# Kernel optimization log

Measured on AMD Instinct MI355X. Metric: run time of the kernel, lower is better.

## Reference

```python
import jax, jax.numpy as jnp
import numpy as np

DIM = 1024
HEADS = 16
HEAD_DIM = DIM // HEADS
K_NEIGH = 64  # local_window, adaptive_window=False
SCALE = 1.0 / np.sqrt(HEAD_DIM)


def setup_inputs() -> dict:
    key = jax.random.key(0)
    ks = jax.random.split(key, 6)
    b, n = 1, 4096
    x = jax.random.normal(ks[0], (b, n, DIM), dtype=jnp.float32)
    cantor_coords = jax.random.uniform(ks[1], (n,), dtype=jnp.float32)
    # torch nn.Linear(dim, 3*dim): weight [3*dim, dim]; we store transposed [dim, 3*dim]
    W_qkv = jax.random.normal(ks[2], (DIM, 3 * DIM), dtype=jnp.float32) * (1.0 / np.sqrt(DIM))
    b_qkv = jax.random.normal(ks[3], (3 * DIM,), dtype=jnp.float32) * 0.01
    W_out = jax.random.normal(ks[4], (DIM, DIM), dtype=jnp.float32) * (1.0 / np.sqrt(DIM))
    b_out = jax.random.normal(ks[5], (DIM,), dtype=jnp.float32) * 0.01
    return {"x": x, "cantor_coords": cantor_coords, "W_qkv": W_qkv,
            "b_qkv": b_qkv, "W_out": W_out, "b_out": b_out}


def _routes(cantor_coords):
    # [n, n] pairwise |c_i - c_j|; k smallest -> top_k of negated distances
    d = jnp.abs(cantor_coords[:, None] - cantor_coords[None, :])
    _, idx = jax.lax.top_k(-d, K_NEIGH)  # [n, k]
    return idx


def reference(x, cantor_coords, W_qkv, b_qkv, W_out, b_out):
    b, n, _ = x.shape
    qkv = x @ W_qkv + b_qkv                          # [b, n, 3*dim]
    qkv = qkv.reshape(b, n, 3, HEADS, HEAD_DIM)
    qkv = jnp.transpose(qkv, (2, 0, 3, 1, 4))        # [3, b, h, n, d]
    q, k, v = qkv[0], qkv[1], qkv[2]

    routes = _routes(cantor_coords)                  # [n, k]
    k_g = k[:, :, routes, :]                         # [b, h, n, k, d]
    v_g = v[:, :, routes, :]
    scores = jnp.einsum('bhqd,bhqkd->bhqk', q, k_g) * SCALE
    attn = jax.nn.softmax(scores, axis=-1)           # dropout p=0 (eval)
    out = jnp.einsum('bhqk,bhqkd->bhqd', attn, v_g)  # [b, h, n, d]
    out = jnp.transpose(out, (0, 2, 1, 3)).reshape(b, n, DIM)
    return out @ W_out + b_out
```

## Files before the change

### kernel.cpp

```cpp
#include <hip/hip_runtime.h>
#include <hip/hip_bf16.h>

typedef _Float16 f16x8 __attribute__((ext_vector_type(8)));
typedef float f32x4 __attribute__((ext_vector_type(4)));
typedef unsigned long long u64;

#define NSEQ 4096
#define DIMM 1024
#define NQKV 3072

#define BAR() asm volatile("s_barrier" ::: "memory")

__device__ __forceinline__ f32x4 mfma16(f16x8 a, f16x8 b, f32x4 c) {
  return __builtin_amdgcn_mfma_f32_16x16x32_f16(a, b, c, 0, 0, 0);
}

__device__ __forceinline__ void glds16(const void* g, void* l) {
  __builtin_amdgcn_global_load_lds(
      (const __attribute__((address_space(1))) void*)g,
      (__attribute__((address_space(3))) void*)l, 16, 0, 0);
}

__global__ __launch_bounds__(256) void prep_kernel(
    const float* __restrict__ x, _Float16* __restrict__ xh,
    const float* __restrict__ Wqkv, _Float16* __restrict__ wqkvt,
    const float* __restrict__ Wout, _Float16* __restrict__ woutt,
    const float* __restrict__ cc, int* __restrict__ sorted_idx,
    float* __restrict__ csort) {
  __shared__ __align__(16) char plds[16640];
  const int bid = blockIdx.x, t = threadIdx.x;
  if (bid < 2048) {
    const int i = bid * 256 + t;
    const float4 a = ((const float4*)x)[i * 2];
    const float4 b = ((const float4*)x)[i * 2 + 1];
    f16x8 o = {(_Float16)a.x, (_Float16)a.y, (_Float16)a.z, (_Float16)a.w,
               (_Float16)b.x, (_Float16)b.y, (_Float16)b.z, (_Float16)b.w};
    ((f16x8*)xh)[i] = o;
  } else if (bid < 3072) {
    const bool qkv = bid < 2816;
    const int sub = qkv ? bid - 2048 : bid - 2816;
    const float* W = qkv ? Wqkv : Wout;
    _Float16* Wt = qkv ? wqkvt : woutt;
    const int Nn = qkv ? 3072 : 1024;
    const int k0 = (sub & 15) * 64, n0 = (sub >> 4) * 64;
    float (*tile)[65] = (float(*)[65])plds;
    const int tx = t & 63, ty = t >> 6;
    for (int rr = ty; rr < 64; rr += 4)
      tile[rr][tx] = W[(size_t)(k0 + rr) * Nn + n0 + tx];
    __syncthreads();
#pragma unroll
    for (int it = 0; it < 2; ++it) {
      const int idx = it * 256 + t;
      const int row = idx >> 3, seg = idx & 7;
      f16x8 v;
#pragma unroll
      for (int j = 0; j < 8; ++j) v[j] = (_Float16)tile[seg * 8 + j][row];
      *(f16x8*)&Wt[(size_t)(n0 + row) * 1024 + k0 + seg * 8] = v;
    }
  } else {
    float* sc = (float*)plds;
#pragma unroll
    for (int it = 0; it < 4; ++it) {
      const int i = it * 256 + t;
      ((float4*)sc)[i] = ((const float4*)cc)[i];
    }
    __syncthreads();
    const int elem = (bid - 3072) * 32 + (t >> 3);
    const int s = t & 7;
    const unsigned mybits = __float_as_uint(sc[elem]);
    int cnt = 0;
#pragma unroll 8
    for (int m = 0; m < 512; ++m) {
      const int j = s + (m << 3);
      const unsigned bj = __float_as_uint(sc[j]);
      cnt += (bj < mybits || (bj == mybits && j < elem)) ? 1 : 0;
    }
    cnt += __shfl_xor(cnt, 1);
    cnt += __shfl_xor(cnt, 2);
    cnt += __shfl_xor(cnt, 4);
    if (s == 0) {
      sorted_idx[cnt] = elem;
      csort[cnt] = sc[elem];
    }
  }
}

__device__ __forceinline__ f16x8 ldsfrag(const char* base, int r, int g) {
  return *(const f16x8*)(base + r * 128 + ((g ^ (r & 7)) << 4));
}

__device__ __forceinline__ void stage_half(const char* gbase, size_t kb, int t,
                                           char* lds_half, int tid) {
#pragma unroll
  for (int s = 0; s < 2; ++s) {
    const int rel = tid * 16 + s * 8192;
    const int r = rel >> 7;
    const int g = (rel >> 4) & 7;
    const int gg = g ^ (r & 7);
    glds16(gbase + (size_t)r * kb + t * 128 + gg * 16, lds_half + rel);
  }
}

__device__ __forceinline__ void stage_64r(const char* gbase, size_t kb, int t,
                                          char* lds8k, int tid) {
  const int rel = tid * 16;
  const int r = rel >> 7;
  const int g = (rel >> 4) & 7;
  const int gg = g ^ (r & 7);
  glds16(gbase + (size_t)r * kb + t * 128 + gg * 16, lds8k + rel);
}

__device__ __forceinline__ void rd_b3(const char* Bb, int wn, int lr, int kg,
                                      f16x8 (&bf)[3][2]) {
#pragma unroll
  for (int nt = 0; nt < 3; ++nt) {
    bf[nt][0] = ldsfrag(Bb, wn + nt * 16 + lr, kg);
    bf[nt][1] = ldsfrag(Bb, wn + nt * 16 + lr, 4 + kg);
  }
}

template <int Q>
__device__ __forceinline__ void rd_a(const char* Ab, int wm, int lr, int kg,
                                     f16x8 (&af)[2][2]) {
#pragma unroll
  for (int m = 0; m < 2; ++m) {
    af[m][0] = ldsfrag(Ab, wm + (2 * Q + m) * 16 + lr, kg);
    af[m][1] = ldsfrag(Ab, wm + (2 * Q + m) * 16 + lr, 4 + kg);
  }
}

template <int Q>
__device__ __forceinline__ void do_mfma3(const f16x8 (&af)[2][2],
                                         const f16x8 (&bf)[3][2],
                                         f32x4 (&acc)[8][3]) {
#pragma unroll
  for (int m = 0; m < 2; ++m)
#pragma unroll
    for (int nt = 0; nt < 3; ++nt) {
      acc[2 * Q + m][nt] = mfma16(af[m][0], bf[nt][0], acc[2 * Q + m][nt]);
      acc[2 * Q + m][nt] = mfma16(af[m][1], bf[nt][1], acc[2 * Q + m][nt]);
    }
}

template <bool LAST>
__device__ __forceinline__ void ktile_pair192(const char* Ag, const char* Bg,
                                              size_t kb, char* smem, int tid,
                                              int wm, int wn, int lr, int kg,
                                              int t1, int t2, int t3,
                                              f32x4 (&acc)[8][3]) {
  char* A0 = smem;
  char* A1 = smem + 32768;
  char* B0 = smem + 65536;
  char* B1 = smem + 65536 + 24576;
  f16x8 bf[3][2], af[2][2];
  rd_b3(B0, wn, lr, kg, bf);
  rd_a<0>(A0, wm, lr, kg, af);
  stage_64r(Ag, kb, t1, A1, tid);
  stage_64r(Ag + 64 * kb, kb, t1, A1 + 8192, tid);
  BAR();
  __builtin_amdgcn_s_setprio(1);
  do_mfma3<0>(af, bf, acc);
  __builtin_amdgcn_s_setprio(0);
  BAR();
  rd_a<1>(A0, wm, lr, kg, af);
  stage_64r(Ag + 128 * kb, kb, t1, A1 + 16384, tid);
  stage_64r(Ag + 192 * kb, kb, t1, A1 + 24576, tid);
  BAR();
  __builtin_amdgcn_s_setprio(1);
  do_mfma3<1>(af, bf, acc);
  __builtin_amdgcn_s_setprio(0);
  BAR();
  rd_a<2>(A0, wm, lr, kg, af);
  if (!LAST) {
    stage_64r(Bg, kb, t2, B0, tid);
    stage_64r(Bg + 64 * kb, kb, t2, B0 + 8192, tid);
  }
  BAR();
  __builtin_amdgcn_s_setprio(1);
  do_mfma3<2>(af, bf, acc);
  __builtin_amdgcn_s_setprio(0);
  BAR();
  rd_a<3>(A0, wm, lr, kg, af);
  if (!LAST) stage_64r(Bg + 128 * kb, kb, t2, B0 + 16384, tid);
  BAR();
  __builtin_amdgcn_s_setprio(1);
  do_mfma3<3>(af, bf, acc);
  __builtin_amdgcn_s_setprio(0);
  if (LAST)
    asm volatile("s_waitcnt vmcnt(0)" ::: "memory");
  else
    asm volatile("s_waitcnt vmcnt(3)" ::: "memory");
  BAR();
  rd_b3(B1, wn, lr, kg, bf);
  rd_a<0>(A1, wm, lr, kg, af);
  if (!LAST) {
    stage_64r(Ag, kb, t2, A0, tid);
    stage_64r(Ag + 64 * kb, kb, t2, A0 + 8192, tid);
  }
  BAR();
  __builtin_amdgcn_s_setprio(1);
  do_mfma3<0>(af, bf, acc);
  __builtin_amdgcn_s_setprio(0);
  BAR();
  rd_a<1>(A1, wm, lr, kg, af);
  if (!LAST) {
    stage_64r(Ag + 128 * kb, kb, t2, A0 + 16384, tid);
    stage_64r(Ag + 192 * kb, kb, t2, A0 + 24576, tid);
  }
  BAR();
  __builtin_amdgcn_s_setprio(1);
  do_mfma3<1>(af, bf, acc);
  __builtin_amdgcn_s_setprio(0);
  BAR();
  rd_a<2>(A1, wm, lr, kg, af);
  if (!LAST) {
    stage_64r(Bg, kb, t3, B1, tid);
    stage_64r(Bg + 64 * kb, kb, t3, B1 + 8192, tid);
  }
  BAR();
  __builtin_amdgcn_s_setprio(1);
  do_mfma3<2>(af, bf, acc);
  __builtin_amdgcn_s_setprio(0);
  BAR();
  rd_a<3>(A1, wm, lr, kg, af);
  if (!LAST) stage_64r(Bg + 128 * kb, kb, t3, B1 + 16384, tid);
  BAR();
  __builtin_amdgcn_s_setprio(1);
  do_mfma3<3>(af, bf, acc);
  __builtin_amdgcn_s_setprio(0);
  if (!LAST) asm volatile("s_waitcnt vmcnt(3)" ::: "memory");
  BAR();
}

__global__ __launch_bounds__(512, 2) void qkvmask_kernel(
    const _Float16* __restrict__ A, const _Float16* __restrict__ Bt,
    const float* __restrict__ bias, _Float16* __restrict__ C,
    const float* __restrict__ csort, const int* __restrict__ sorted_idx,
    unsigned* __restrict__ masks) {
  extern __shared__ char smem[];
  const int tid = threadIdx.x;
  const int lane = tid & 63, wid = tid >> 6;
  if (blockIdx.x >= 256) {
    const int p = (blockIdx.x - 256) * 8 + wid;
    int W0 = 64 * (p >> 6) - 64;
    W0 = min(max(W0, 0), NSEQ - 192);
    const float cp = csort[p];
    u64 key[4];
#pragma unroll
    for (int r = 0; r < 3; ++r) {
      const int w = r * 64 + lane;
      const float d = fabsf(csort[W0 + w] - cp);
      key[r] = (((u64)__float_as_uint(d)) << 20) |
               (((u64)(unsigned)sorted_idx[W0 + w]) << 8) | (unsigned)w;
    }
    key[3] = ~0ull;
#pragma unroll
    for (int k = 2; k <= 256; k <<= 1) {
#pragma unroll
      for (int j = k >> 1; j > 0; j >>= 1) {
        if (j >= 64) {
          const int rj = j >> 6;
#pragma unroll
          for (int r = 0; r < 4; ++r) {
            const int rp = r ^ rj;
            if (rp > r) {
              const bool up = (((r * 64) & k) == 0);
              const u64 a = key[r], b2 = key[rp];
              const bool sw = (a > b2) == up;
              key[r] = sw ? b2 : a;
              key[rp] = sw ? a : b2;
            }
          }
        } else {
#pragma unroll
          for (int r = 0; r < 4; ++r) {
            const u64 pv = __shfl_xor(key[r], j);
            const bool up = (((r * 64 + lane) & k) == 0);
            const bool lower = ((lane & j) == 0);
            const bool takemin = (lower == up);
            const u64 mn = key[r] < pv ? key[r] : pv;
            const u64 mx = key[r] < pv ? pv : key[r];
            key[r] = takemin ? mn : mx;
          }
        }
      }
    }
    const unsigned w0 = (unsigned)(key[0] & 0xffu);
    const unsigned hi = w0 >> 5, bit = 1u << (w0 & 31u);
    unsigned m0w = hi == 0 ? bit : 0u;
    unsigned m1w = hi == 1 ? bit : 0u;
    unsigned m2w = hi == 2 ? bit : 0u;
    unsigned m3w = hi == 3 ? bit : 0u;
    unsigned m4w = hi == 4 ? bit : 0u;
    unsigned m5w = hi == 5 ? bit : 0u;
#pragma unroll
    for (int s = 1; s < 64; s <<= 1) {
      m0w |= __shfl_xor(m0w, s);
      m1w |= __shfl_xor(m1w, s);
      m2w |= __shfl_xor(m2w, s);
      m3w |= __shfl_xor(m3w, s);
      m4w |= __shfl_xor(m4w, s);
      m5w |= __shfl_xor(m5w, s);
    }
    if (lane < 8) {
      unsigned val = 0u;
      val = lane == 0 ? m0w : val;
      val = lane == 1 ? m1w : val;
      val = lane == 2 ? m2w : val;
      val = lane == 3 ? m3w : val;
      val = lane == 4 ? m4w : val;
      val = lane == 5 ? m5w : val;
      masks[p * 8 + lane] = val;
    }
    return;
  }
  const int NN = 3072;
  const size_t kb = 2048;
  const int lr = lane & 15, kg = lane >> 4;
  const int wm = (wid >> 2) * 128, wn = (wid & 3) * 48;
  const int bid = blockIdx.x;
  const int flat = (bid & 7) * 32 + (bid >> 3);
  const int bx = flat >> 4, by = flat & 15;
  const int m0 = bx * 256, n0 = by * 192;
  const char* Ag = (const char*)A + (size_t)m0 * kb;
  const char* Bg = (const char*)Bt + (size_t)n0 * kb;
  char* A0 = smem;
  char* B0 = smem + 65536;
  char* B1 = smem + 65536 + 24576;
  f32x4 acc[8][3] = {};
#pragma unroll
  for (int u = 0; u < 4; ++u)
    stage_64r(Ag + (size_t)(64 * u) * kb, kb, 0, A0 + u * 8192, tid);
#pragma unroll
  for (int u = 0; u < 3; ++u)
    stage_64r(Bg + (size_t)(64 * u) * kb, kb, 0, B0 + u * 8192, tid);
#pragma unroll
  for (int u = 0; u < 3; ++u)
    stage_64r(Bg + (size_t)(64 * u) * kb, kb, 1, B1 + u * 8192, tid);
  asm volatile("s_waitcnt vmcnt(3)" ::: "memory");
  BAR();
#pragma unroll 1
  for (int i = 0; i < 7; ++i)
    ktile_pair192<false>(Ag, Bg, kb, smem, tid, wm, wn, lr, kg, 2 * i + 1,
                         2 * i + 2, 2 * i + 3, acc);
  ktile_pair192<true>(Ag, Bg, kb, smem, tid, wm, wn, lr, kg, 15, 16, 17, acc);
#pragma unroll
  for (int nt = 0; nt < 3; ++nt) {
    const int col = n0 + wn + nt * 16 + lr;
    const float bv = bias[col];
#pragma unroll
    for (int mt = 0; mt < 8; ++mt) {
      const int row0 = m0 + wm + mt * 16 + kg * 4;
#pragma unroll
      for (int rr = 0; rr < 4; ++rr)
        C[(size_t)(row0 + rr) * NN + col] = (_Float16)(acc[mt][nt][rr] + bv);
    }
  }
}

__global__ __launch_bounds__(512, 2) void out_gemm128_kernel(
    const _Float16* __restrict__ A, const _Float16* __restrict__ Bt,
    const float* __restrict__ bias, float* __restrict__ C) {
  extern __shared__ char smem[];
  const size_t kb = 2048;
  const int tid = threadIdx.x;
  const int lane = tid & 63, wid = tid >> 6;
  const int lr = lane & 15, kg = lane >> 4;
  const int wm = (wid >> 2) * 64, wn = (wid & 3) * 32;
  const int bid = blockIdx.x;
  const int flat = (bid & 7) * 32 + (bid >> 3);
  const int bx = flat >> 3, by = flat & 7;
  const int m0 = bx * 128, n0 = by * 128;
  const char* Ag = (const char*)A + (size_t)m0 * kb;
  const char* Bg = (const char*)Bt + (size_t)n0 * kb;
  f32x4 acc[4][2] = {};
  stage_half(Ag, kb, 0, smem, tid);
  stage_half(Bg, kb, 0, smem + 49152, tid);
  stage_half(Ag, kb, 1, smem + 16384, tid);
  stage_half(Bg, kb, 1, smem + 49152 + 16384, tid);
  asm volatile("s_waitcnt vmcnt(4)" ::: "memory");
  BAR();
#pragma unroll
  for (int t = 0; t < 16; ++t) {
    const char* At = smem + (t % 3) * 16384;
    const char* Bb = smem + 49152 + (t % 3) * 16384;
    f16x8 bf[2][2], af[4][2];
#pragma unroll
    for (int nt = 0; nt < 2; ++nt) {
      bf[nt][0] = ldsfrag(Bb, wn + nt * 16 + lr, kg);
      bf[nt][1] = ldsfrag(Bb, wn + nt * 16 + lr, 4 + kg);
    }
#pragma unroll
    for (int m = 0; m < 4; ++m) {
      af[m][0] = ldsfrag(At, wm + m * 16 + lr, kg);
      af[m][1] = ldsfrag(At, wm + m * 16 + lr, 4 + kg);
    }
    if (t < 14) {
      stage_half(Ag, kb, t + 2, smem + ((t + 2) % 3) * 16384, tid);
      stage_half(Bg, kb, t + 2, smem + 49152 + ((t + 2) % 3) * 16384, tid);
    }
    BAR();
    __builtin_amdgcn_s_setprio(1);
#pragma unroll
    for (int m = 0; m < 4; ++m)
#pragma unroll
      for (int nt = 0; nt < 2; ++nt) {
        acc[m][nt] = mfma16(af[m][0], bf[nt][0], acc[m][nt]);
        acc[m][nt] = mfma16(af[m][1], bf[nt][1], acc[m][nt]);
      }
    __builtin_amdgcn_s_setprio(0);
    if (t < 14)
      asm volatile("s_waitcnt vmcnt(4)" ::: "memory");
    else if (t == 14)
      asm volatile("s_waitcnt vmcnt(0)" ::: "memory");
    BAR();
  }
#pragma unroll
  for (int nt = 0; nt < 2; ++nt) {
    const int col = n0 + wn + nt * 16 + lr;
    const float bv = bias[col];
#pragma unroll
    for (int mt = 0; mt < 4; ++mt) {
      const int row0 = m0 + wm + mt * 16 + kg * 4;
#pragma unroll
      for (int rr = 0; rr < 4; ++rr)
        C[(size_t)(row0 + rr) * 1024 + col] = acc[mt][nt][rr] + bv;
    }
  }
}

__global__ __launch_bounds__(256) void attn_kernel(
    const _Float16* __restrict__ qkvh, const unsigned* __restrict__ masks,
    const int* __restrict__ sorted_idx, _Float16* __restrict__ attn_h) {
  __shared__ __align__(128) char sK[24576];
  __shared__ __align__(128) char sV[24576];
  const int flat = (blockIdx.x & 7) * 128 + (blockIdx.x >> 3);
  const int b = flat & 63, h = flat >> 6;
  const int tid = threadIdx.x, lane = tid & 63, wid = tid >> 6;
  const int W0 = min(max(64 * b - 64, 0), NSEQ - 192);
  const int lrow16 = lane & 15, kgrp = lane >> 4;
  int ridx[6];
#pragma unroll
  for (int c = 0; c < 6; ++c)
    ridx[c] = sorted_idx[W0 + c * 32 + wid * 8 + (lane >> 3)];
#pragma unroll
  for (int c = 0; c < 6; ++c) {
    const int o = c * 4096 + wid * 1024 + lane * 16;
    const int row = o >> 7;
    const int inrow = (o & 127) ^ ((row & 7) << 4);
    glds16((const char*)qkvh + (size_t)ridx[c] * 6144 + 2048 + h * 128 + inrow,
           sK + o);
  }
  f16x8 vreg[6];
#pragma unroll
  for (int c = 0; c < 6; ++c) {
    const int o = c * 4096 + wid * 1024 + lane * 16;
    vreg[c] = *(const f16x8*)((const char*)qkvh + (size_t)ridx[c] * 6144 +
                              4096 + h * 128 + (o & 127));
  }
  const int p_base = b * 64 + wid * 16;
  const int orig_q = sorted_idx[p_base + lrow16];
  const char* qp = (const char*)qkvh + (size_t)orig_q * 6144 + h * 128 + kgrp * 16;
  const f16x8 aq0 = *(const f16x8*)qp;
  const f16x8 aq1 = *(const f16x8*)(qp + 64);
  unsigned mb[4];
#pragma unroll
  for (int r = 0; r < 4; ++r) {
    const int p = p_base + kgrp * 4 + r;
    const uint4 wa = *(const uint4*)&masks[p * 8];
    const uint2 wb2 = *(const uint2*)&masks[p * 8 + 4];
    const unsigned wsv6[6] = {wa.x, wa.y, wa.z, wa.w, wb2.x, wb2.y};
    unsigned bits = 0;
#pragma unroll
    for (int n = 0; n < 12; ++n)
      bits |= ((wsv6[n >> 1] >> (((n & 1) << 4) + lrow16)) & 1u) << n;
    mb[r] = bits;
  }
  const int lrot = lane & 7;
#pragma unroll
  for (int c = 0; c < 6; ++c) {
    const int o = c * 4096 + wid * 1024 + lane * 16;
    const int k = o >> 7;
    const int d0 = (o & 127) >> 1;
#pragma unroll
    for (int ee = 0; ee < 8; ++ee) {
      const int e = (ee + lrot) & 7;
      const int d = d0 + e;
      *(_Float16*)(sV + d * 384 + ((2 * k) ^ ((d & 7) << 4))) = vreg[c][e];
    }
  }
  __syncthreads();
  float sv[12][4];
#pragma unroll
  for (int n = 0; n < 12; ++n) {
    const int j = n * 16 + lrow16;
    const int sw = (j & 7) << 4;
    const char* kr = sK + j * 128;
    const f16x8 b0 = *(const f16x8*)(kr + ((kgrp * 16) ^ sw));
    const f16x8 b1 = *(const f16x8*)(kr + ((64 + kgrp * 16) ^ sw));
    f32x4 a = {};
    a = mfma16(aq0, b0, a);
    a = mfma16(aq1, b1, a);
#pragma unroll
    for (int r = 0; r < 4; ++r)
      sv[n][r] = ((mb[r] >> n) & 1u) ? a[r] * 0.125f : -1e30f;
  }
#pragma unroll
  for (int r = 0; r < 4; ++r) {
    float m = sv[0][r];
#pragma unroll
    for (int n = 1; n < 12; ++n) m = fmaxf(m, sv[n][r]);
    m = fmaxf(m, __shfl_xor(m, 1));
    m = fmaxf(m, __shfl_xor(m, 2));
    m = fmaxf(m, __shfl_xor(m, 4));
    m = fmaxf(m, __shfl_xor(m, 8));
    float s = 0.f;
#pragma unroll
    for (int n = 0; n < 12; ++n) {
      const float e = __expf(sv[n][r] - m);
      sv[n][r] = e;
      s += e;
    }
    s += __shfl_xor(s, 1);
    s += __shfl_xor(s, 2);
    s += __shfl_xor(s, 4);
    s += __shfl_xor(s, 8);
    const float rinv = 1.f / s;
#pragma unroll
    for (int n = 0; n < 12; ++n) sv[n][r] *= rinv;
  }
  __syncthreads();
#pragma unroll
  for (int n = 0; n < 12; ++n) {
#pragma unroll
    for (int r = 0; r < 4; ++r) {
      const int lrw = wid * 16 + kgrp * 4 + r;
      const int cb = (n * 16 + lrow16) * 2;
      *(_Float16*)(sK + lrw * 384 + (cb ^ ((lrw & 7) << 4))) = (_Float16)sv[n][r];
    }
  }
  __syncthreads();
  f32x4 oacc[4] = {};
  const int arow = wid * 16 + lrow16;
  const int swa = (arow & 7) << 4;
#pragma unroll
  for (int kt = 0; kt < 6; ++kt) {
    const int kbo = kt * 64 + kgrp * 16;
    const f16x8 pa = *(const f16x8*)(sK + arow * 384 + (kbo ^ swa));
#pragma unroll
    for (int nt = 0; nt < 4; ++nt) {
      const int d = nt * 16 + lrow16;
      const f16x8 vb = *(const f16x8*)(sV + d * 384 + (kbo ^ ((d & 7) << 4)));
      oacc[nt] = mfma16(pa, vb, oacc[nt]);
    }
  }
#pragma unroll
  for (int r = 0; r < 4; ++r) {
    const int p = p_base + kgrp * 4 + r;
    const int orig = sorted_idx[p];
    _Float16* op = attn_h + (size_t)orig * DIMM + h * 64;
#pragma unroll
    for (int nt = 0; nt < 4; ++nt)
      op[nt * 16 + lrow16] = (_Float16)oacc[nt][r];
  }
}

extern "C" void kernel_launch(void* const* d_in, const int* in_sizes, int n_in,
                              void* d_out, int out_size, void* d_ws, size_t ws_size,
                              hipStream_t stream) {
  const float* x = (const float*)d_in[0];
  const float* cc = (const float*)d_in[1];
  const float* Wqkv = (const float*)d_in[2];
  const float* bqkv = (const float*)d_in[3];
  const float* Wout = (const float*)d_in[4];
  const float* bout = (const float*)d_in[5];
  char* ws = (char*)d_ws;

  _Float16* xh = (_Float16*)(ws + 0);
  _Float16* wqkvt = (_Float16*)(ws + 8388608);
  _Float16* woutt = (_Float16*)(ws + 14680064);
  _Float16* qkvh = (_Float16*)(ws + 16777216);
  _Float16* atnh = (_Float16*)(ws + 41943040);
  int* sidx = (int*)(ws + 50331648);
  float* csort = (float*)(ws + 50348032);
  unsigned* msk = (unsigned*)(ws + 50364416);

  hipFuncSetAttribute((const void*)qkvmask_kernel,
                      hipFuncAttributeMaxDynamicSharedMemorySize, 114688);
  hipFuncSetAttribute((const void*)out_gemm128_kernel,
                      hipFuncAttributeMaxDynamicSharedMemorySize, 98304);

  prep_kernel<<<3200, 256, 0, stream>>>(x, xh, Wqkv, wqkvt, Wout, woutt, cc,
                                        sidx, csort);
  qkvmask_kernel<<<768, 512, 114688, stream>>>(xh, wqkvt, bqkv, qkvh, csort,
                                               sidx, msk);
  attn_kernel<<<1024, 256, 0, stream>>>(qkvh, msk, sidx, atnh);
  out_gemm128_kernel<<<256, 512, 98304, stream>>>(atnh, woutt, bout,
                                                  (float*)d_out);
}
```

Before: 102.0 us.

## Enlarge QKV GEMM tile to 256x256 and double per-block mask work

The QKV projection GEMM tile grows from 256x192 to 256x256, giving 192 GEMM blocks instead of 256, with each wave holding 8x4 accumulator tiles and B staged in 32 KB halves. The neighbour-mask blocks now process 16 positions each over two iterations, so 256 mask blocks replace 512 and the grid shrinks from 768 to 448. The aim is better arithmetic intensity per loaded byte and fewer block launches. In exchange, LDS per block rises to 128 KB, which may lower occupancy, and more accumulator registers are needed. 192 blocks may also underfill the GPU's compute units.

```diff
diff --git a/kernel.cpp b/kernel.cpp
--- a/kernel.cpp
+++ b/kernel.cpp
@@ -101,27 +101,18 @@
   }
 }
 
-__device__ __forceinline__ void stage_64r(const char* gbase, size_t kb, int t,
-                                          char* lds8k, int tid) {
-  const int rel = tid * 16;
-  const int r = rel >> 7;
-  const int g = (rel >> 4) & 7;
-  const int gg = g ^ (r & 7);
-  glds16(gbase + (size_t)r * kb + t * 128 + gg * 16, lds8k + rel);
-}
-
-__device__ __forceinline__ void rd_b3(const char* Bb, int wn, int lr, int kg,
-                                      f16x8 (&bf)[3][2]) {
-#pragma unroll
-  for (int nt = 0; nt < 3; ++nt) {
+__device__ __forceinline__ void rd_b4(const char* Bb, int wn, int lr, int kg,
+                                      f16x8 (&bf)[4][2]) {
+#pragma unroll
+  for (int nt = 0; nt < 4; ++nt) {
     bf[nt][0] = ldsfrag(Bb, wn + nt * 16 + lr, kg);
     bf[nt][1] = ldsfrag(Bb, wn + nt * 16 + lr, 4 + kg);
   }
 }
 
 template <int Q>
-__device__ __forceinline__ void rd_a(const char* Ab, int wm, int lr, int kg,
-                                     f16x8 (&af)[2][2]) {
+__device__ __forceinline__ void rd_a2(const char* Ab, int wm, int lr, int kg,
+                                      f16x8 (&af)[2][2]) {
 #pragma unroll
   for (int m = 0; m < 2; ++m) {
     af[m][0] = ldsfrag(Ab, wm + (2 * Q + m) * 16 + lr, kg);
@@ -130,105 +121,91 @@
 }
 
 template <int Q>
-__device__ __forceinline__ void do_mfma3(const f16x8 (&af)[2][2],
-                                         const f16x8 (&bf)[3][2],
-                                         f32x4 (&acc)[8][3]) {
+__device__ __forceinline__ void do_mfma4(const f16x8 (&af)[2][2],
+                                         const f16x8 (&bf)[4][2],
+                                         f32x4 (&acc)[8][4]) {
 #pragma unroll
   for (int m = 0; m < 2; ++m)
 #pragma unroll
-    for (int nt = 0; nt < 3; ++nt) {
+    for (int nt = 0; nt < 4; ++nt) {
       acc[2 * Q + m][nt] = mfma16(af[m][0], bf[nt][0], acc[2 * Q + m][nt]);
       acc[2 * Q + m][nt] = mfma16(af[m][1], bf[nt][1], acc[2 * Q + m][nt]);
     }
 }
 
 template <bool LAST>
-__device__ __forceinline__ void ktile_pair192(const char* Ag, const char* Bg,
+__device__ __forceinline__ void ktile_pair256(const char* Ag, const char* Bg,
                                               size_t kb, char* smem, int tid,
                                               int wm, int wn, int lr, int kg,
                                               int t1, int t2, int t3,
-                                              f32x4 (&acc)[8][3]) {
+                                              f32x4 (&acc)[8][4]) {
   char* A0 = smem;
   char* A1 = smem + 32768;
   char* B0 = smem + 65536;
-  char* B1 = smem + 65536 + 24576;
-  f16x8 bf[3][2], af[2][2];
-  rd_b3(B0, wn, lr, kg, bf);
-  rd_a<0>(A0, wm, lr, kg, af);
-  stage_64r(Ag, kb, t1, A1, tid);
-  stage_64r(Ag + 64 * kb, kb, t1, A1 + 8192, tid);
-  BAR();
-  __builtin_amdgcn_s_setprio(1);
-  do_mfma3<0>(af, bf, acc);
-  __builtin_amdgcn_s_setprio(0);
-  BAR();
-  rd_a<1>(A0, wm, lr, kg, af);
-  stage_64r(Ag + 128 * kb, kb, t1, A1 + 16384, tid);
-  stage_64r(Ag + 192 * kb, kb, t1, A1 + 24576, tid);
-  BAR();
-  __builtin_amdgcn_s_setprio(1);
-  do_mfma3<1>(af, bf, acc);
-  __builtin_amdgcn_s_setprio(0);
-  BAR();
-  rd_a<2>(A0, wm, lr, kg, af);
-  if (!LAST) {
-    stage_64r(Bg, kb, t2, B0, tid);
-    stage_64r(Bg + 64 * kb, kb, t2, B0 + 8192, tid);
-  }
-  BAR();
-  __builtin_amdgcn_s_setprio(1);
-  do_mfma3<2>(af, bf, acc);
-  __builtin_amdgcn_s_setprio(0);
-  BAR();
-  rd_a<3>(A0, wm, lr, kg, af);
-  if (!LAST) stage_64r(Bg + 128 * kb, kb, t2, B0 + 16384, tid);
-  BAR();
-  __builtin_amdgcn_s_setprio(1);
-  do_mfma3<3>(af, bf, acc);
+  char* B1 = smem + 98304;
+  f16x8 bf[4][2], af[2][2];
+  rd_b4(B0, wn, lr, kg, bf);
+  rd_a2<0>(A0, wm, lr, kg, af);
+  stage_half(Ag, kb, t1, A1, tid);
+  BAR();
+  __builtin_amdgcn_s_setprio(1);
+  do_mfma4<0>(af, bf, acc);
+  __builtin_amdgcn_s_setprio(0);
+  BAR();
+  rd_a2<1>(A0, wm, lr, kg, af);
+  stage_half(Ag + 128 * kb, kb, t1, A1 + 16384, tid);
+  BAR();
+  __builtin_amdgcn_s_setprio(1);
+  do_mfma4<1>(af, bf, acc);
+  __builtin_amdgcn_s_setprio(0);
+  BAR();
+  rd_a2<2>(A0, wm, lr, kg, af);
+  if (!LAST) stage_half(Bg, kb, t2, B0, tid);
+  BAR();
+  __builtin_amdgcn_s_setprio(1);
+  do_mfma4<2>(af, bf, acc);
+  __builtin_amdgcn_s_setprio(0);
+  BAR();
+  rd_a2<3>(A0, wm, lr, kg, af);
+  if (!LAST) stage_half(Bg + 128 * kb, kb, t2, B0 + 16384, tid);
+  BAR();
+  __builtin_amdgcn_s_setprio(1);
+  do_mfma4<3>(af, bf, acc);
   __builtin_amdgcn_s_setprio(0);
   if (LAST)
     asm volatile("s_waitcnt vmcnt(0)" ::: "memory");
   else
-    asm volatile("s_waitcnt vmcnt(3)" ::: "memory");
-  BAR();
-  rd_b3(B1, wn, lr, kg, bf);
-  rd_a<0>(A1, wm, lr, kg, af);
-  if (!LAST) {
-    stage_64r(Ag, kb, t2, A0, tid);
-    stage_64r(Ag + 64 * kb, kb, t2, A0 + 8192, tid);
-  }
-  BAR();
-  __builtin_amdgcn_s_setprio(1);
-  do_mfma3<0>(af, bf, acc);
-  __builtin_amdgcn_s_setprio(0);
-  BAR();
-  rd_a<1>(A1, wm, lr, kg, af);
-  if (!LAST) {
-    stage_64r(Ag + 128 * kb, kb, t2, A0 + 16384, tid);
-    stage_64r(Ag + 192 * kb, kb, t2, A0 + 24576, tid);
-  }
-  BAR();
-  __builtin_amdgcn_s_setprio(1);
-  do_mfma3<1>(af, bf, acc);
-  __builtin_amdgcn_s_setprio(0);
-  BAR();
-  rd_a<2>(A1, wm, lr, kg, af);
-  if (!LAST) {
-    stage_64r(Bg, kb, t3, B1, tid);
-    stage_64r(Bg + 64 * kb, kb, t3, B1 + 8192, tid);
-  }
-  BAR();
-  __builtin_amdgcn_s_setprio(1);
-  do_mfma3<2>(af, bf, acc);
-  __builtin_amdgcn_s_setprio(0);
-  BAR();
-  rd_a<3>(A1, wm, lr, kg, af);
-  if (!LAST) stage_64r(Bg + 128 * kb, kb, t3, B1 + 16384, tid);
-  BAR();
-  __builtin_amdgcn_s_setprio(1);
-  do_mfma3<3>(af, bf, acc);
-  __builtin_amdgcn_s_setprio(0);
-  if (!LAST) asm volatile("s_waitcnt vmcnt(3)" ::: "memory");
+    asm volatile("s_waitcnt vmcnt(4)" ::: "memory");
+  BAR();
+  rd_b4(B1, wn, lr, kg, bf);
+  rd_a2<0>(A1, wm, lr, kg, af);
+  if (!LAST) stage_half(Ag, kb, t2, A0, tid);
+  BAR();
+  __builtin_amdgcn_s_setprio(1);
+  do_mfma4<0>(af, bf, acc);
+  __builtin_amdgcn_s_setprio(0);
+  BAR();
+  rd_a2<1>(A1, wm, lr, kg, af);
+  if (!LAST) stage_half(Ag + 128 * kb, kb, t2, A0 + 16384, tid);
+  BAR();
+  __builtin_amdgcn_s_setprio(1);
+  do_mfma4<1>(af, bf, acc);
+  __builtin_amdgcn_s_setprio(0);
+  BAR();
+  rd_a2<2>(A1, wm, lr, kg, af);
+  if (!LAST) stage_half(Bg, kb, t3, B1, tid);
+  BAR();
+  __builtin_amdgcn_s_setprio(1);
+  do_mfma4<2>(af, bf, acc);
+  __builtin_amdgcn_s_setprio(0);
+  BAR();
+  rd_a2<3>(A1, wm, lr, kg, af);
+  if (!LAST) stage_half(Bg + 128 * kb, kb, t3, B1 + 16384, tid);
+  BAR();
+  __builtin_amdgcn_s_setprio(1);
+  do_mfma4<3>(af, bf, acc);
+  __builtin_amdgcn_s_setprio(0);
+  if (!LAST) asm volatile("s_waitcnt vmcnt(4)" ::: "memory");
   BAR();
 }
 
@@ -240,112 +217,112 @@
   extern __shared__ char smem[];
   const int tid = threadIdx.x;
   const int lane = tid & 63, wid = tid >> 6;
-  if (blockIdx.x >= 256) {
-    const int p = (blockIdx.x - 256) * 8 + wid;
-    int W0 = 64 * (p >> 6) - 64;
-    W0 = min(max(W0, 0), NSEQ - 192);
-    const float cp = csort[p];
-    u64 key[4];
-#pragma unroll
-    for (int r = 0; r < 3; ++r) {
-      const int w = r * 64 + lane;
-      const float d = fabsf(csort[W0 + w] - cp);
-      key[r] = (((u64)__float_as_uint(d)) << 20) |
-               (((u64)(unsigned)sorted_idx[W0 + w]) << 8) | (unsigned)w;
-    }
-    key[3] = ~0ull;
-#pragma unroll
-    for (int k = 2; k <= 256; k <<= 1) {
-#pragma unroll
-      for (int j = k >> 1; j > 0; j >>= 1) {
-        if (j >= 64) {
-          const int rj = j >> 6;
-#pragma unroll
-          for (int r = 0; r < 4; ++r) {
-            const int rp = r ^ rj;
-            if (rp > r) {
-              const bool up = (((r * 64) & k) == 0);
-              const u64 a = key[r], b2 = key[rp];
-              const bool sw = (a > b2) == up;
-              key[r] = sw ? b2 : a;
-              key[rp] = sw ? a : b2;
+  if (blockIdx.x >= 192) {
+#pragma unroll 1
+    for (int it = 0; it < 2; ++it) {
+      const int p = (blockIdx.x - 192) * 16 + it * 8 + wid;
+      int W0 = 64 * (p >> 6) - 64;
+      W0 = min(max(W0, 0), NSEQ - 192);
+      const float cp = csort[p];
+      u64 key[4];
+#pragma unroll
+      for (int r = 0; r < 3; ++r) {
+        const int w = r * 64 + lane;
+        const float d = fabsf(csort[W0 + w] - cp);
+        key[r] = (((u64)__float_as_uint(d)) << 20) |
+                 (((u64)(unsigned)sorted_idx[W0 + w]) << 8) | (unsigned)w;
+      }
+      key[3] = ~0ull;
+#pragma unroll
+      for (int k = 2; k <= 256; k <<= 1) {
+#pragma unroll
+        for (int j = k >> 1; j > 0; j >>= 1) {
+          if (j >= 64) {
+            const int rj = j >> 6;
+#pragma unroll
+            for (int r = 0; r < 4; ++r) {
+              const int rp = r ^ rj;
+              if (rp > r) {
+                const bool up = (((r * 64) & k) == 0);
+                const u64 a = key[r], b2 = key[rp];
+                const bool sw = (a > b2) == up;
+                key[r] = sw ? b2 : a;
+                key[rp] = sw ? a : b2;
+              }
             }
-          }
-        } else {
-#pragma unroll
-          for (int r = 0; r < 4; ++r) {
-            const u64 pv = __shfl_xor(key[r], j);
-            const bool up = (((r * 64 + lane) & k) == 0);
-            const bool lower = ((lane & j) == 0);
-            const bool takemin = (lower == up);
-            const u64 mn = key[r] < pv ? key[r] : pv;
-            const u64 mx = key[r] < pv ? pv : key[r];
-            key[r] = takemin ? mn : mx;
+          } else {
+#pragma unroll
+            for (int r = 0; r < 4; ++r) {
+              const u64 pv = __shfl_xor(key[r], j);
+              const bool up = (((r * 64 + lane) & k) == 0);
+              const bool lower = ((lane & j) == 0);
+              const bool takemin = (lower == up);
+              const u64 mn = key[r] < pv ? key[r] : pv;
+              const u64 mx = key[r] < pv ? pv : key[r];
+              key[r] = takemin ? mn : mx;
+            }
           }
         }
       }
-    }
-    const unsigned w0 = (unsigned)(key[0] & 0xffu);
-    const unsigned hi = w0 >> 5, bit = 1u << (w0 & 31u);
-    unsigned m0w = hi == 0 ? bit : 0u;
-    unsigned m1w = hi == 1 ? bit : 0u;
-    unsigned m2w = hi == 2 ? bit : 0u;
-    unsigned m3w = hi == 3 ? bit : 0u;
-    unsigned m4w = hi == 4 ? bit : 0u;
-    unsigned m5w = hi == 5 ? bit : 0u;
-#pragma unroll
-    for (int s = 1; s < 64; s <<= 1) {
-      m0w |= __shfl_xor(m0w, s);
-      m1w |= __shfl_xor(m1w, s);
-      m2w |= __shfl_xor(m2w, s);
-      m3w |= __shfl_xor(m3w, s);
-      m4w |= __shfl_xor(m4w, s);
-      m5w |= __shfl_xor(m5w, s);
-    }
-    if (lane < 8) {
-      unsigned val = 0u;
-      val = lane == 0 ? m0w : val;
-      val = lane == 1 ? m1w : val;
-      val = lane == 2 ? m2w : val;
-      val = lane == 3 ? m3w : val;
-      val = lane == 4 ? m4w : val;
-      val = lane == 5 ? m5w : val;
-      masks[p * 8 + lane] = val;
+      const unsigned w0 = (unsigned)(key[0] & 0xffu);
+      const unsigned hi = w0 >> 5, bit = 1u << (w0 & 31u);
+      unsigned m0w = hi == 0 ? bit : 0u;
+      unsigned m1w = hi == 1 ? bit : 0u;
+      unsigned m2w = hi == 2 ? bit : 0u;
+      unsigned m3w = hi == 3 ? bit : 0u;
+      unsigned m4w = hi == 4 ? bit : 0u;
+      unsigned m5w = hi == 5 ? bit : 0u;
+#pragma unroll
+      for (int s = 1; s < 64; s <<= 1) {
+        m0w |= __shfl_xor(m0w, s);
+        m1w |= __shfl_xor(m1w, s);
+        m2w |= __shfl_xor(m2w, s);
+        m3w |= __shfl_xor(m3w, s);
+        m4w |= __shfl_xor(m4w, s);
+        m5w |= __shfl_xor(m5w, s);
+      }
+      if (lane < 8) {
+        unsigned val = 0u;
+        val = lane == 0 ? m0w : val;
+        val = lane == 1 ? m1w : val;
+        val = lane == 2 ? m2w : val;
+        val = lane == 3 ? m3w : val;
+        val = lane == 4 ? m4w : val;
+        val = lane == 5 ? m5w : val;
+        masks[p * 8 + lane] = val;
+      }
     }
     return;
   }
   const int NN = 3072;
   const size_t kb = 2048;
   const int lr = lane & 15, kg = lane >> 4;
-  const int wm = (wid >> 2) * 128, wn = (wid & 3) * 48;
+  const int wm = (wid >> 2) * 128, wn = (wid & 3) * 64;
   const int bid = blockIdx.x;
-  const int flat = (bid & 7) * 32 + (bid >> 3);
-  const int bx = flat >> 4, by = flat & 15;
-  const int m0 = bx * 256, n0 = by * 192;
+  const int flat = (bid & 7) * 24 + (bid >> 3);
+  const int bx = flat / 12, by = flat % 12;
+  const int m0 = bx * 256, n0 = by * 256;
   const char* Ag = (const char*)A + (size_t)m0 * kb;
   const char* Bg = (const char*)Bt + (size_t)n0 * kb;
   char* A0 = smem;
   char* B0 = smem + 65536;
-  char* B1 = smem + 65536 + 24576;
-  f32x4 acc[8][3] = {};
-#pragma unroll
-  for (int u = 0; u < 4; ++u)
-    stage_64r(Ag + (size_t)(64 * u) * kb, kb, 0, A0 + u * 8192, tid);
-#pragma unroll
-  for (int u = 0; u < 3; ++u)
-    stage_64r(Bg + (size_t)(64 * u) * kb, kb, 0, B0 + u * 8192, tid);
-#pragma unroll
-  for (int u = 0; u < 3; ++u)
-    stage_64r(Bg + (size_t)(64 * u) * kb, kb, 1, B1 + u * 8192, tid);
-  asm volatile("s_waitcnt vmcnt(3)" ::: "memory");
+  char* B1 = smem + 98304;
+  f32x4 acc[8][4] = {};
+  stage_half(Ag, kb, 0, A0, tid);
+  stage_half(Ag + 128 * kb, kb, 0, A0 + 16384, tid);
+  stage_half(Bg, kb, 0, B0, tid);
+  stage_half(Bg + 128 * kb, kb, 0, B0 + 16384, tid);
+  stage_half(Bg, kb, 1, B1, tid);
+  stage_half(Bg + 128 * kb, kb, 1, B1 + 16384, tid);
+  asm volatile("s_waitcnt vmcnt(4)" ::: "memory");
   BAR();
 #pragma unroll 1
   for (int i = 0; i < 7; ++i)
-    ktile_pair192<false>(Ag, Bg, kb, smem, tid, wm, wn, lr, kg, 2 * i + 1,
+    ktile_pair256<false>(Ag, Bg, kb, smem, tid, wm, wn, lr, kg, 2 * i + 1,
                          2 * i + 2, 2 * i + 3, acc);
-  ktile_pair192<true>(Ag, Bg, kb, smem, tid, wm, wn, lr, kg, 15, 16, 17, acc);
-#pragma unroll
-  for (int nt = 0; nt < 3; ++nt) {
+  ktile_pair256<true>(Ag, Bg, kb, smem, tid, wm, wn, lr, kg, 15, 16, 17, acc);
+#pragma unroll
+  for (int nt = 0; nt < 4; ++nt) {
     const int col = n0 + wn + nt * 16 + lr;
     const float bv = bias[col];
 #pragma unroll
@@ -586,13 +563,13 @@
   unsigned* msk = (unsigned*)(ws + 50364416);
 
   hipFuncSetAttribute((const void*)qkvmask_kernel,
-                      hipFuncAttributeMaxDynamicSharedMemorySize, 114688);
+                      hipFuncAttributeMaxDynamicSharedMemorySize, 131072);
   hipFuncSetAttribute((const void*)out_gemm128_kernel,
                       hipFuncAttributeMaxDynamicSharedMemorySize, 98304);
 
   prep_kernel<<<3200, 256, 0, stream>>>(x, xh, Wqkv, wqkvt, Wout, woutt, cc,
                                         sidx, csort);
-  qkvmask_kernel<<<768, 512, 114688, stream>>>(xh, wqkvt, bqkv, qkvh, csort,
+  qkvmask_kernel<<<448, 512, 131072, stream>>>(xh, wqkvt, bqkv, qkvh, csort,
                                                sidx, msk);
   attn_kernel<<<1024, 256, 0, stream>>>(qkvh, msk, sidx, atnh);
   out_gemm128_kernel<<<256, 512, 98304, stream>>>(atnh, woutt, bout,
```

Result: slower. 105.5 us (+3.5%).
